# Performance work log

Hardware: AMD Instinct MI355X
Metric: run time of the kernel (lower is better)

The kernel has to match this reference:

```python
import jax, jax.numpy as jnp
import numpy as np

B, T, C, H = 4, 2048, 1024, 16
D = C // H  # head_dim = 64
ROPE_BASE = 10000.0
EPS = 1e-6


def _rms_norm(x):
    return x / jnp.sqrt(jnp.mean(x * x, axis=-1, keepdims=True) + EPS)


def _rope_tables(t_len, d, dtype):
    inv_freq = 1.0 / (ROPE_BASE ** (jnp.arange(0, d, 2, dtype=jnp.float32) / d))
    t = jnp.arange(t_len, dtype=jnp.float32)
    freqs = jnp.outer(t, inv_freq)  # [T, D/2]
    return jnp.cos(freqs).astype(dtype)[None, None], jnp.sin(freqs).astype(dtype)[None, None]


def _apply_rotary(x, cos, sin):
    d = x.shape[-1] // 2
    x1, x2 = x[..., :d], x[..., d:]
    return jnp.concatenate([x1 * cos + x2 * sin, -x1 * sin + x2 * cos], axis=-1)


def setup_inputs() -> dict:
    key = jax.random.key(0)
    k1, k2, k3, k4, k5 = jax.random.split(key, 5)
    x = jax.random.normal(k1, (B, T, C), dtype=jnp.float32)
    Wqkv = jax.random.normal(k2, (C, 3 * C), dtype=jnp.float32) * 0.02
    bqkv = jax.random.normal(k3, (3 * C,), dtype=jnp.float32) * 0.02
    # NOTE: original zero-inits c_proj.weight; randomized here for a non-trivial baseline.
    Wproj = jax.random.normal(k4, (C, C), dtype=jnp.float32) * 0.02
    bproj = jax.random.normal(k5, (C,), dtype=jnp.float32) * 0.02
    lamb = jnp.float32(0.5)
    return {"x": x, "Wqkv": Wqkv, "bqkv": bqkv, "Wproj": Wproj, "bproj": bproj, "lamb": lamb}


def reference(x, Wqkv, bqkv, Wproj, bproj, lamb):
    b, t, c = x.shape
    qkv = x @ Wqkv + bqkv  # [B,T,3C]
    q, k, v = jnp.split(qkv, 3, axis=-1)
    # [B,T,C] -> [B,H,T,D]
    to_heads = lambda z: z.reshape(b, t, H, D).transpose(0, 2, 1, 3)
    query, key_, value = to_heads(q), to_heads(k), to_heads(v)
    # v1 defaults to value -> blend is identity, kept for faithfulness
    value = (1.0 - lamb) * value + lamb * value
    query = _rms_norm(query)
    key_ = _rms_norm(key_)
    cos, sin = _rope_tables(t, D, x.dtype)
    query = _apply_rotary(query, cos, sin)
    key_ = _apply_rotary(key_, cos, sin)
    # causal SDPA
    scale = 1.0 / jnp.sqrt(jnp.float32(D)).astype(x.dtype)
    scores = jnp.einsum('bhqd,bhkd->bhqk', query, key_) * scale
    causal = jnp.tril(jnp.ones((t, t), dtype=bool))
    scores = jnp.where(causal[None, None], scores, jnp.finfo(scores.dtype).min)
    probs = jax.nn.softmax(scores, axis=-1)
    attn = jnp.einsum('bhqk,bhkd->bhqd', probs, value)
    attn = attn.transpose(0, 2, 1, 3).reshape(b, t, c)
    out = attn @ Wproj + bproj
    return out, value
```

## Files before the change

kernel.cpp:

```cpp
#include <hip/hip_runtime.h>
#include <math.h>

#define B_   4
#define T_   2048
#define C_   1024
#define H_   16
#define D_   64
#define TC3  3072

typedef __attribute__((ext_vector_type(8))) short short8;
typedef __attribute__((ext_vector_type(4))) short short4b;
typedef __attribute__((ext_vector_type(8))) unsigned short ushortv8;
typedef __attribute__((ext_vector_type(4))) float f32x4;

__device__ __forceinline__ float bf2f(unsigned short u) {
  unsigned int x = ((unsigned int)u) << 16;
  float f; __builtin_memcpy(&f, &x, 4); return f;
}
__device__ __forceinline__ unsigned short f2bf(float f) {
  unsigned int x; __builtin_memcpy(&x, &f, 4);
  x += 0x7fff + ((x >> 16) & 1);
  return (unsigned short)(x >> 16);
}

#define MFMA32(a, b, c) __builtin_amdgcn_mfma_f32_16x16x32_bf16(a, b, c, 0, 0, 0)
#if __has_builtin(__builtin_amdgcn_mfma_f32_16x16x16_bf16)
#define MFMA16(a, b, c) __builtin_amdgcn_mfma_f32_16x16x16_bf16(a, b, c, 0, 0, 0)
#else
#define MFMA16(a, b, c) __builtin_amdgcn_mfma_f32_16x16x16bf16_1k(a, b, c, 0, 0, 0)
#endif

#define GLOAD_LDS(gp, lp) __builtin_amdgcn_global_load_lds( \
    (const __attribute__((address_space(1))) unsigned int*)(gp), \
    (__attribute__((address_space(3))) unsigned int*)(lp), 16, 0, 0)

__global__ __launch_bounds__(256)
void convert_bf16(const float* __restrict__ x, unsigned short* __restrict__ xb) {
  const size_t i = ((size_t)blockIdx.x * 256 + threadIdx.x) * 8;
  float4 f0 = *(const float4*)(x + i);
  float4 f1 = *(const float4*)(x + i + 4);
  ushortv8 u = { f2bf(f0.x), f2bf(f0.y), f2bf(f0.z), f2bf(f0.w),
                 f2bf(f1.x), f2bf(f1.y), f2bf(f1.z), f2bf(f1.w) };
  *(ushortv8*)(xb + i) = u;
}

__global__ __launch_bounds__(256)
void transpose_bf16(const float* __restrict__ W, unsigned short* __restrict__ WT,
                    int K, int N) {
  __shared__ float tile[64][65];
  const int k0 = blockIdx.y * 64, n0 = blockIdx.x * 64;
  const int r = threadIdx.x >> 4, c4 = (threadIdx.x & 15) * 4;
#pragma unroll
  for (int p = 0; p < 4; ++p) {
    int kk = p * 16 + r;
    float4 v = *(const float4*)(W + (size_t)(k0 + kk) * N + n0 + c4);
    tile[kk][c4 + 0] = v.x; tile[kk][c4 + 1] = v.y;
    tile[kk][c4 + 2] = v.z; tile[kk][c4 + 3] = v.w;
  }
  __syncthreads();
#pragma unroll
  for (int p = 0; p < 4; ++p) {
    int nn = p * 16 + r;
    ushort4 o = { f2bf(tile[c4 + 0][nn]), f2bf(tile[c4 + 1][nn]),
                  f2bf(tile[c4 + 2][nn]), f2bf(tile[c4 + 3][nn]) };
    *(ushort4*)(WT + (size_t)(n0 + nn) * K + k0 + c4) = o;
  }
}

template<bool OUT_BF16>
__global__ __launch_bounds__(256)
void gemm_mfma(const unsigned short* __restrict__ Ab,
               const unsigned short* __restrict__ Bt,
               const float* __restrict__ bias, void* __restrict__ Cv,
               int K, int lda, int ldb, int ldc) {
  __shared__ unsigned short As[128 * 64];
  __shared__ unsigned short Bs[128 * 64];
  const int tid = threadIdx.x;
  const int l = tid & 63, w = tid >> 6;
  const int m0 = blockIdx.y * 128, n0 = blockIdx.x * 128;
  const int wm = (w & 1) * 64, wn = (w >> 1) * 64;
  const int fr = l & 15, g = l >> 4;

  f32x4 acc[4][4];
#pragma unroll
  for (int i = 0; i < 4; ++i)
#pragma unroll
    for (int j = 0; j < 4; ++j) acc[i][j] = (f32x4)0.f;

  const int gr = l >> 3;
  const int gc = (l & 7) ^ gr;

  for (int kt = 0; kt < K; kt += 64) {
    __syncthreads();
#pragma unroll
    for (int q = 0; q < 4; ++q) {
      int rr = (w * 4 + q) * 8 + gr;
      GLOAD_LDS(Ab + (size_t)(m0 + rr) * lda + kt + gc * 8,
                &As[(w * 4 + q) * 512]);
      GLOAD_LDS(Bt + (size_t)(n0 + rr) * ldb + kt + gc * 8,
                &Bs[(w * 4 + q) * 512]);
    }
    __syncthreads();

#pragma unroll
    for (int s = 0; s < 2; ++s) {
      const int cofs = (((s * 4 + g) ^ (fr & 7)) << 3);
      short8 a[4], b[4];
#pragma unroll
      for (int i = 0; i < 4; ++i)
        a[i] = *(const short8*)&As[(wm + i * 16 + fr) * 64 + cofs];
#pragma unroll
      for (int j = 0; j < 4; ++j)
        b[j] = *(const short8*)&Bs[(wn + j * 16 + fr) * 64 + cofs];
#pragma unroll
      for (int i = 0; i < 4; ++i)
#pragma unroll
        for (int j = 0; j < 4; ++j)
          acc[i][j] = MFMA32(a[i], b[j], acc[i][j]);
    }
  }

#pragma unroll
  for (int j = 0; j < 4; ++j) {
    const int n = n0 + wn + j * 16 + fr;
    const float bv = bias[n];
#pragma unroll
    for (int i = 0; i < 4; ++i) {
#pragma unroll
      for (int rg = 0; rg < 4; ++rg) {
        const int m = m0 + wm + i * 16 + g * 4 + rg;
        float v = acc[i][j][rg] + bv;
        if (OUT_BF16) ((unsigned short*)Cv)[(size_t)m * ldc + n] = f2bf(v);
        else          ((float*)Cv)[(size_t)m * ldc + n] = v;
      }
    }
  }
}

__global__ __launch_bounds__(256)
void rmsrope_kernel(unsigned short* __restrict__ qkv) {
  const int unit = blockIdx.x * 4 + (threadIdx.x >> 6);
  const int lane = threadIdx.x & 63;
  const int b = unit / (T_ * H_);
  const int rem = unit % (T_ * H_);
  const int t = rem / H_;
  const int h = rem % H_;
  const size_t base = (size_t)(b * T_ + t) * TC3;

  const int i = lane & 31;
  const float inv = __builtin_amdgcn_exp2f(-13.2877123795494f * (float)(2 * i)
                                           * (1.0f / 64.0f));
  const float ang = (float)t * inv;
  const float cs = cosf(ang);
  const float sn = sinf(ang);

  {
    const size_t idx = base + h * 64 + lane;
    float q = bf2f(qkv[idx]);
    float ss = q * q;
    ss += __shfl_xor(ss, 32); ss += __shfl_xor(ss, 16);
    ss += __shfl_xor(ss, 8);  ss += __shfl_xor(ss, 4);
    ss += __shfl_xor(ss, 2);  ss += __shfl_xor(ss, 1);
    float qn = q * (1.0f / sqrtf(ss * (1.0f / 64.0f) + 1e-6f));
    float part = __shfl_xor(qn, 32);
    float out = (lane < 32) ? (qn * cs + part * sn) : (qn * cs - part * sn);
    qkv[idx] = f2bf(out);
  }
  {
    const size_t idx = base + C_ + h * 64 + lane;
    float k = bf2f(qkv[idx]);
    float ss = k * k;
    ss += __shfl_xor(ss, 32); ss += __shfl_xor(ss, 16);
    ss += __shfl_xor(ss, 8);  ss += __shfl_xor(ss, 4);
    ss += __shfl_xor(ss, 2);  ss += __shfl_xor(ss, 1);
    float kn = k * (1.0f / sqrtf(ss * (1.0f / 64.0f) + 1e-6f));
    float part = __shfl_xor(kn, 32);
    float out = (lane < 32) ? (kn * cs + part * sn) : (kn * cs - part * sn);
    qkv[idx] = f2bf(out);
  }
}

__global__ __launch_bounds__(256)
void vtrans_kernel(const unsigned short* __restrict__ qkv,
                   const float* __restrict__ lambp,
                   unsigned short* __restrict__ vT,
                   float* __restrict__ valOut) {
  __shared__ float tile[64][65];
  const int t0 = blockIdx.x * 64;
  const int head = blockIdx.y;
  const int b = head >> 4, h = head & 15;
  const float lamb = lambp[0];
  const int r = threadIdx.x >> 4, c4 = (threadIdx.x & 15) * 4;
#pragma unroll
  for (int p = 0; p < 4; ++p) {
    int tt = p * 16 + r;
    ushort4 raw = *(const ushort4*)(
        qkv + (size_t)(b * T_ + t0 + tt) * TC3 + 2 * C_ + h * 64 + c4);
    float4 f;
    f.x = (1.f - lamb) * bf2f(raw.x) + lamb * bf2f(raw.x);
    f.y = (1.f - lamb) * bf2f(raw.y) + lamb * bf2f(raw.y);
    f.z = (1.f - lamb) * bf2f(raw.z) + lamb * bf2f(raw.z);
    f.w = (1.f - lamb) * bf2f(raw.w) + lamb * bf2f(raw.w);
    tile[tt][c4 + 0] = f.x; tile[tt][c4 + 1] = f.y;
    tile[tt][c4 + 2] = f.z; tile[tt][c4 + 3] = f.w;
    *(float4*)(valOut + ((size_t)head * T_ + t0 + tt) * D_ + c4) = f;
  }
  __syncthreads();
#pragma unroll
  for (int p = 0; p < 4; ++p) {
    int d = p * 16 + r;
    ushort4 o = { f2bf(tile[c4 + 0][d]), f2bf(tile[c4 + 1][d]),
                  f2bf(tile[c4 + 2][d]), f2bf(tile[c4 + 3][d]) };
    *(ushort4*)(vT + ((size_t)head * D_ + d) * T_ + t0 + c4) = o;
  }
}

#define SCL_ (0.125f * 1.44269504088896f)

template<bool MASKED>
__device__ __forceinline__ void attn_tile(
    const unsigned short* __restrict__ Ks,
    const unsigned short* __restrict__ Vs,
    const short8 (&qf)[2][2], int qrow0 , int k0,
    int fr, int quad, int f8,
    float (&l_pt)[2], f32x4 (&o)[2][4]) {
  f32x4 st[2][4];
#pragma unroll
  for (int i = 0; i < 2; ++i)
#pragma unroll
    for (int j = 0; j < 4; ++j) st[i][j] = (f32x4)0.f;

#pragma unroll
  for (int kc = 0; kc < 2; ++kc) {
    const int cofs = (((kc * 4 + quad) ^ f8) << 3);
#pragma unroll
    for (int j = 0; j < 4; ++j) {
      short8 kf = *(const short8*)&Ks[(j * 16 + fr) * 64 + cofs];
      st[0][j] = MFMA32(kf, qf[kc][0], st[0][j]);
      st[1][j] = MFMA32(kf, qf[kc][1], st[1][j]);
    }
  }

  short4b pa[2][4];
#pragma unroll
  for (int i = 0; i < 2; ++i) {
    const int qg = qrow0 + i * 16 + fr;
#pragma unroll
    for (int j = 0; j < 4; ++j) {
      const int kg = k0 + j * 16 + quad * 4;
#pragma unroll
      for (int r = 0; r < 4; ++r) {
        float arg = st[i][j][r] * SCL_;
        if (MASKED) { if (kg + r > qg) arg = -INFINITY; }
        float p = __builtin_amdgcn_exp2f(arg);
        l_pt[i] += p;
        st[i][j][r] = p;
      }
      pa[i][j] = (short4b){ (short)f2bf(st[i][j][0]), (short)f2bf(st[i][j][1]),
                            (short)f2bf(st[i][j][2]), (short)f2bf(st[i][j][3]) };
    }
  }

#pragma unroll
  for (int c = 0; c < 4; ++c) {
    const int vofs = ((((c * 2 + (quad >> 1)) ^ f8) << 3) + (quad & 1) * 4);
#pragma unroll
    for (int jd = 0; jd < 4; ++jd) {
      short4b vf = *(const short4b*)&Vs[(jd * 16 + fr) * 64 + vofs];
      o[0][jd] = MFMA16(pa[0][c], vf, o[0][jd]);
      o[1][jd] = MFMA16(pa[1][c], vf, o[1][jd]);
    }
  }
}

__device__ __forceinline__ void attn_store(
    unsigned short* __restrict__ qkv, int bT, int h, int qrow0,
    int fr, int quad, float (&l_pt)[2], f32x4 (&o)[2][4]) {
#pragma unroll
  for (int i = 0; i < 2; ++i) {
    float lv = l_pt[i];
    lv += __shfl_xor(lv, 16);
    lv += __shfl_xor(lv, 32);
    float inv = 1.0f / lv;
    float invq[4];
#pragma unroll
    for (int r = 0; r < 4; ++r) invq[r] = __shfl(inv, quad * 4 + r);
#pragma unroll
    for (int jd = 0; jd < 4; ++jd) {
      const int d = jd * 16 + fr;
#pragma unroll
      for (int r = 0; r < 4; ++r) {
        const int row = qrow0 + i * 16 + quad * 4 + r;
        qkv[(size_t)(bT + row) * TC3 + 2 * C_ + h * 64 + d] =
            f2bf(o[i][jd][r] * invq[r]);
      }
    }
  }
}

__global__ __launch_bounds__(256)
void flash_mfma(unsigned short* __restrict__ qkv,
                const unsigned short* __restrict__ vT) {
  __shared__ unsigned short Qs[2][128 * 64];
  __shared__ unsigned short Ks[64 * 64];
  __shared__ unsigned short Vs[64 * 64];

  const int qa = blockIdx.x;
  const int qb = 15 - qa;
  const int b  = blockIdx.z;
  const int h  = blockIdx.y;
  const int bT = b * T_;

  const int tid = threadIdx.x;
  const int w = tid >> 6, l = tid & 63;
  const int fr = l & 15, quad = l >> 4;
  const int gr = l >> 3;
  const int gc = (l & 7) ^ gr;
  const int f8 = fr & 7;

#pragma unroll
  for (int s = 0; s < 4; ++s) {
    int row = w * 32 + s * 8 + gr;
    GLOAD_LDS(qkv + (size_t)(bT + qa * 128 + row) * TC3 + h * 64 + gc * 8,
              &Qs[0][(w * 32 + s * 8) * 64]);
    GLOAD_LDS(qkv + (size_t)(bT + qb * 128 + row) * TC3 + h * 64 + gc * 8,
              &Qs[1][(w * 32 + s * 8) * 64]);
  }
  __syncthreads();

  short8 qfa[2][2], qfb[2][2];
#pragma unroll
  for (int kc = 0; kc < 2; ++kc) {
    const int cofs = (((kc * 4 + quad) ^ f8) << 3);
    qfa[kc][0] = *(const short8*)&Qs[0][(w * 32 + fr) * 64 + cofs];
    qfa[kc][1] = *(const short8*)&Qs[0][(w * 32 + 16 + fr) * 64 + cofs];
    qfb[kc][0] = *(const short8*)&Qs[1][(w * 32 + fr) * 64 + cofs];
    qfb[kc][1] = *(const short8*)&Qs[1][(w * 32 + 16 + fr) * 64 + cofs];
  }

  float la[2] = {0.f, 0.f}, lb[2] = {0.f, 0.f};
  f32x4 oa[2][4], ob[2][4];
#pragma unroll
  for (int i = 0; i < 2; ++i)
#pragma unroll
    for (int j = 0; j < 4; ++j) { oa[i][j] = (f32x4)0.f; ob[i][j] = (f32x4)0.f; }

  const int nka = 2 * qa + 2;
  const int nkb = 2 * qb + 2;
  const int qra = qa * 128 + w * 32;
  const int qrb = qb * 128 + w * 32;

  for (int kt = 0; kt < nkb; ++kt) {
    const int k0 = kt * 64;
    __syncthreads();
#pragma unroll
    for (int s = 0; s < 2; ++s) {
      int row = w * 16 + s * 8;
      GLOAD_LDS(qkv + (size_t)(bT + k0 + row + gr) * TC3 + C_ + h * 64 + gc * 8,
                &Ks[row * 64]);
      GLOAD_LDS(vT + ((size_t)(b * H_ + h) * D_ + row + gr) * T_ + k0 + gc * 8,
                &Vs[row * 64]);
    }
    __syncthreads();

    if (kt < nka) {
      if (kt >= nka - 2)
        attn_tile<true >(Ks, Vs, qfa, qra, k0, fr, quad, f8, la, oa);
      else
        attn_tile<false>(Ks, Vs, qfa, qra, k0, fr, quad, f8, la, oa);
    }
    if (kt >= nkb - 2)
      attn_tile<true >(Ks, Vs, qfb, qrb, k0, fr, quad, f8, lb, ob);
    else
      attn_tile<false>(Ks, Vs, qfb, qrb, k0, fr, quad, f8, lb, ob);
  }

  attn_store(qkv, bT, h, qra, fr, quad, la, oa);
  attn_store(qkv, bT, h, qrb, fr, quad, lb, ob);
}

extern "C" void kernel_launch(void* const* d_in, const int* in_sizes, int n_in,
                              void* d_out, int out_size, void* d_ws, size_t ws_size,
                              hipStream_t stream) {
  const float* x     = (const float*)d_in[0];
  const float* Wqkv  = (const float*)d_in[1];
  const float* bqkv  = (const float*)d_in[2];
  const float* Wproj = (const float*)d_in[3];
  const float* bproj = (const float*)d_in[4];
  const float* lamb  = (const float*)d_in[5];

  float* out     = (float*)d_out;
  float* val_out = out + (size_t)B_ * T_ * C_;

  unsigned short* qkvb   = (unsigned short*)d_ws;
  unsigned short* WqkvT  = qkvb + (size_t)B_ * T_ * TC3;
  unsigned short* WprojT = WqkvT + (size_t)TC3 * C_;
  unsigned short* vT     = WprojT + (size_t)C_ * C_;
  unsigned short* xb     = vT + (size_t)B_ * H_ * D_ * T_;

  convert_bf16<<<dim3((B_ * T_ * C_) / 2048), 256, 0, stream>>>(x, xb);
  transpose_bf16<<<dim3(TC3 / 64, C_ / 64), 256, 0, stream>>>(Wqkv, WqkvT, C_, TC3);
  transpose_bf16<<<dim3(C_ / 64, C_ / 64), 256, 0, stream>>>(Wproj, WprojT, C_, C_);

  gemm_mfma<true><<<dim3(TC3 / 128, (B_ * T_) / 128), 256, 0, stream>>>(
      xb, WqkvT, bqkv, qkvb, C_, C_, C_, TC3);

  rmsrope_kernel<<<dim3((B_ * T_ * H_) / 4), 256, 0, stream>>>(qkvb);

  vtrans_kernel<<<dim3(T_ / 64, B_ * H_), 256, 0, stream>>>(qkvb, lamb, vT, val_out);

  flash_mfma<<<dim3(8, H_, B_), 256, 0, stream>>>(qkvb, vT);

  gemm_mfma<false><<<dim3(C_ / 128, (B_ * T_) / 128), 256, 0, stream>>>(
      qkvb + 2 * C_, WprojT, bproj, out, C_, TC3, C_, C_);
}
```

Before: 341.2 us.

## Split paired causal query tiles into one tile per attention block

The flash attention kernel stops processing a complementary pair of query tiles (qa, 15-qa) per block and gives each block a single 128-row query tile, doubling the grid to 1024 blocks. Tile order is permuted per batch index so long and short causal tiles are interleaved across the launch. The aim is more parallelism, fewer live registers and less LDS per block, which should raise occupancy. The cost is that each K/V tile is now loaded once per query tile instead of being shared by the pair, and per-block work becomes uneven.

```diff
diff --git a/kernel.cpp b/kernel.cpp
--- a/kernel.cpp
+++ b/kernel.cpp
@@ -301,19 +301,21 @@
 __global__ __launch_bounds__(256)
 void flash_mfma(unsigned short* __restrict__ qkv,
                 const unsigned short* __restrict__ vT) {
-  __shared__ unsigned short Qs[2][128 * 64];
+  __shared__ unsigned short Qs[128 * 64];
   __shared__ unsigned short Ks[64 * 64];
   __shared__ unsigned short Vs[64 * 64];
 
-  const int qa = blockIdx.x;
-  const int qb = 15 - qa;
-  const int b  = blockIdx.z;
+  const int z = blockIdx.z;
+  const int xx = ((int)blockIdx.x + ((z >> 1) << 3)) & 15;
+  const int qt = (z & 1) ? (15 - xx) : xx;
+  const int b  = z;
   const int h  = blockIdx.y;
   const int bT = b * T_;
 
   const int tid = threadIdx.x;
   const int w = tid >> 6, l = tid & 63;
   const int fr = l & 15, quad = l >> 4;
+  const int q0 = qt * 128;
   const int gr = l >> 3;
   const int gc = (l & 7) ^ gr;
   const int f8 = fr & 7;
@@ -321,36 +323,30 @@
 #pragma unroll
   for (int s = 0; s < 4; ++s) {
     int row = w * 32 + s * 8 + gr;
-    GLOAD_LDS(qkv + (size_t)(bT + qa * 128 + row) * TC3 + h * 64 + gc * 8,
-              &Qs[0][(w * 32 + s * 8) * 64]);
-    GLOAD_LDS(qkv + (size_t)(bT + qb * 128 + row) * TC3 + h * 64 + gc * 8,
-              &Qs[1][(w * 32 + s * 8) * 64]);
+    GLOAD_LDS(qkv + (size_t)(bT + q0 + row) * TC3 + h * 64 + gc * 8,
+              &Qs[(w * 32 + s * 8) * 64]);
   }
   __syncthreads();
 
-  short8 qfa[2][2], qfb[2][2];
+  short8 qf[2][2];
 #pragma unroll
   for (int kc = 0; kc < 2; ++kc) {
     const int cofs = (((kc * 4 + quad) ^ f8) << 3);
-    qfa[kc][0] = *(const short8*)&Qs[0][(w * 32 + fr) * 64 + cofs];
-    qfa[kc][1] = *(const short8*)&Qs[0][(w * 32 + 16 + fr) * 64 + cofs];
-    qfb[kc][0] = *(const short8*)&Qs[1][(w * 32 + fr) * 64 + cofs];
-    qfb[kc][1] = *(const short8*)&Qs[1][(w * 32 + 16 + fr) * 64 + cofs];
-  }
-
-  float la[2] = {0.f, 0.f}, lb[2] = {0.f, 0.f};
-  f32x4 oa[2][4], ob[2][4];
+    qf[kc][0] = *(const short8*)&Qs[(w * 32 + fr) * 64 + cofs];
+    qf[kc][1] = *(const short8*)&Qs[(w * 32 + 16 + fr) * 64 + cofs];
+  }
+
+  float l_pt[2] = {0.f, 0.f};
+  f32x4 o[2][4];
 #pragma unroll
   for (int i = 0; i < 2; ++i)
 #pragma unroll
-    for (int j = 0; j < 4; ++j) { oa[i][j] = (f32x4)0.f; ob[i][j] = (f32x4)0.f; }
-
-  const int nka = 2 * qa + 2;
-  const int nkb = 2 * qb + 2;
-  const int qra = qa * 128 + w * 32;
-  const int qrb = qb * 128 + w * 32;
-
-  for (int kt = 0; kt < nkb; ++kt) {
+    for (int j = 0; j < 4; ++j) o[i][j] = (f32x4)0.f;
+
+  const int nk = 2 * qt + 2;
+  const int qr0 = q0 + w * 32;
+
+  for (int kt = 0; kt < nk; ++kt) {
     const int k0 = kt * 64;
     __syncthreads();
 #pragma unroll
@@ -363,20 +359,13 @@
     }
     __syncthreads();
 
-    if (kt < nka) {
-      if (kt >= nka - 2)
-        attn_tile<true >(Ks, Vs, qfa, qra, k0, fr, quad, f8, la, oa);
-      else
-        attn_tile<false>(Ks, Vs, qfa, qra, k0, fr, quad, f8, la, oa);
-    }
-    if (kt >= nkb - 2)
-      attn_tile<true >(Ks, Vs, qfb, qrb, k0, fr, quad, f8, lb, ob);
+    if (kt < nk - 2)
+      attn_tile<false>(Ks, Vs, qf, qr0, k0, fr, quad, f8, l_pt, o);
     else
-      attn_tile<false>(Ks, Vs, qfb, qrb, k0, fr, quad, f8, lb, ob);
-  }
-
-  attn_store(qkv, bT, h, qra, fr, quad, la, oa);
-  attn_store(qkv, bT, h, qrb, fr, quad, lb, ob);
+      attn_tile<true >(Ks, Vs, qf, qr0, k0, fr, quad, f8, l_pt, o);
+  }
+
+  attn_store(qkv, bT, h, qr0, fr, quad, l_pt, o);
 }
 
 extern "C" void kernel_launch(void* const* d_in, const int* in_sizes, int n_in,
@@ -409,7 +398,7 @@
 
   vtrans_kernel<<<dim3(T_ / 64, B_ * H_), 256, 0, stream>>>(qkvb, lamb, vT, val_out);
 
-  flash_mfma<<<dim3(8, H_, B_), 256, 0, stream>>>(qkvb, vT);
+  flash_mfma<<<dim3(16, H_, B_), 256, 0, stream>>>(qkvb, vT);
 
   gemm_mfma<false><<<dim3(C_ / 128, (B_ * T_) / 128), 256, 0, stream>>>(
       qkvb + 2 * C_, WprojT, bproj, out, C_, TC3, C_, C_);
```

Result: no change. 334.6 us (-1.9%).
